# Kernel tuning notes

Measured on AMD Instinct MI355X. Metric: run time of the kernel, lower is better.

The kernel has to match this reference:

```python
import jax, jax.numpy as jnp
import numpy as np

N = 20000
DEG = 16
E = N * DEG
IN_DIM = 512
OUT_DIM = 512
H = 4
D = OUT_DIM // H            # head_dim = 128
POS_DIM = 3
M_ROPE = D // (POS_DIM * 2) # 21
D_ROPE = POS_DIM * 2 * M_ROPE  # 126 (2 trailing dims unrotated)
ROPE_BASE = 10000.0

INV_FREQ = jnp.exp(-jnp.arange(M_ROPE, dtype=jnp.float32) * (np.log(ROPE_BASE) / M_ROPE))


def _rope(t, pos):
    # t: (N, D, H), pos: (N, POS_DIM)
    n = t.shape[0]
    angles = pos[:, :, None] * INV_FREQ[None, None, :]        # (N, POS_DIM, M)
    cos = jnp.cos(angles)[..., None]                           # (N, POS_DIM, M, 1)
    sin = jnp.sin(angles)[..., None]
    part = t[:, :D_ROPE, :].reshape(n, POS_DIM, M_ROPE, 2, H)
    even, odd = part[..., 0, :], part[..., 1, :]
    rot_even = even * cos - odd * sin
    rot_odd = even * sin + odd * cos
    rot = jnp.stack((rot_even, rot_odd), axis=3).reshape(n, D_ROPE, H)
    return jnp.concatenate([rot, t[:, D_ROPE:, :]], axis=1)


def setup_inputs() -> dict:
    key = jax.random.key(0)
    ks = jax.random.split(key, 12)
    x = jax.random.normal(ks[0], (N, IN_DIM), jnp.float32)
    pos = jax.random.uniform(ks[1], (N, POS_DIM), jnp.float32) * 100.0
    rows = jnp.repeat(jnp.arange(N, dtype=jnp.int32), DEG)  # sorted, every node has DEG out-edges
    cols = jax.random.randint(ks[2], (E,), 0, N, dtype=jnp.int32)
    s = 1.0 / np.sqrt(IN_DIM)
    Wq = jax.random.normal(ks[3], (OUT_DIM, IN_DIM), jnp.float32) * s
    Wk = jax.random.normal(ks[4], (OUT_DIM, IN_DIM), jnp.float32) * s
    Wv = jax.random.normal(ks[5], (OUT_DIM, IN_DIM), jnp.float32) * s
    Wo = jax.random.normal(ks[6], (OUT_DIM, OUT_DIM), jnp.float32) * s
    bq = jax.random.normal(ks[7], (OUT_DIM,), jnp.float32) * 0.01
    bk = jax.random.normal(ks[8], (OUT_DIM,), jnp.float32) * 0.01
    bv = jax.random.normal(ks[9], (OUT_DIM,), jnp.float32) * 0.01
    bo = jax.random.normal(ks[10], (OUT_DIM,), jnp.float32) * 0.01
    return {"x": x, "pos": pos, "rows": rows, "cols": cols,
            "Wq": Wq, "bq": bq, "Wk": Wk, "bk": bk, "Wv": Wv, "bv": bv, "Wo": Wo, "bo": bo}


def reference(x, pos, rows, cols, Wq, bq, Wk, bk, Wv, bv, Wo, bo):
    n = x.shape[0]
    q = (x @ Wq.T + bq).reshape(n, D, H)
    k = (x @ Wk.T + bk).reshape(n, D, H)
    v = (x @ Wv.T + bv).reshape(n, D, H)
    # scaling by sqrt(k.size(1)) == sqrt(head_dim)
    q = q / jnp.sqrt(jnp.asarray(D, q.dtype))
    q = _rope(q, pos)
    k = _rope(k, pos)
    # per-edge scores: s[e,h] = sum_d q[rows[e],d,h] * k[cols[e],d,h]
    scores = jnp.einsum('edh,edh->eh', q[rows], k[cols])  # (E, H)
    # row-wise sparse softmax per head
    row_max = jax.ops.segment_max(scores, rows, num_segments=n, indices_are_sorted=True)
    p = jnp.exp(scores - row_max[rows])
    denom = jax.ops.segment_sum(p, rows, num_segments=n, indices_are_sorted=True)
    attn = p / denom[rows]                                 # (E, H)
    # bspmm: y[i,d,h] = sum_{e: rows[e]=i} attn[e,h] * v[cols[e],d,h]
    y = jax.ops.segment_sum(attn[:, None, :] * v[cols], rows, num_segments=n, indices_are_sorted=True)
    out = y.reshape(n, OUT_DIM) @ Wo.T + bo
    return out
```

## Files before the change

kernel.cpp:

```cpp
#include <hip/hip_runtime.h>
#include <hip/hip_bf16.h>

#define NN 20000
#define DEG 16
#define KD 512
#define OD 512
#define NH 4
#define DH 128
#define DROPE 126

#define BM 128
#define BN 128
#define BK 64

typedef unsigned short u16;
typedef unsigned int u32;
typedef __attribute__((ext_vector_type(8))) short short8;
typedef __attribute__((ext_vector_type(4))) float f32x4;

__device__ __forceinline__ float b2f(u16 u){ return __uint_as_float((u32)u << 16); }
__device__ __forceinline__ u16 f2b(float f){
  u32 x = __float_as_uint(f);
  return (u16)((x + 0x7fffu + ((x >> 16) & 1u)) >> 16);
}
__device__ __forceinline__ void up8(uint4 u, float* f){
  f[0]=__uint_as_float(u.x<<16); f[1]=__uint_as_float(u.x&0xffff0000u);
  f[2]=__uint_as_float(u.y<<16); f[3]=__uint_as_float(u.y&0xffff0000u);
  f[4]=__uint_as_float(u.z<<16); f[5]=__uint_as_float(u.z&0xffff0000u);
  f[6]=__uint_as_float(u.w<<16); f[7]=__uint_as_float(u.w&0xffff0000u);
}
__device__ __forceinline__ uint4 cvt8(const float* s){
  uint4 a = *(const uint4*)s;
  uint4 b = *(const uint4*)(s + 4);
  uint4 o;
  o.x = (u32)f2b(__uint_as_float(a.x)) | ((u32)f2b(__uint_as_float(a.y)) << 16);
  o.y = (u32)f2b(__uint_as_float(a.z)) | ((u32)f2b(__uint_as_float(a.w)) << 16);
  o.z = (u32)f2b(__uint_as_float(b.x)) | ((u32)f2b(__uint_as_float(b.y)) << 16);
  o.w = (u32)f2b(__uint_as_float(b.z)) | ((u32)f2b(__uint_as_float(b.w)) << 16);
  return o;
}

__device__ __forceinline__ void load_lds16(const u16* g, u16* l) {
  __builtin_amdgcn_global_load_lds(
      (const __attribute__((address_space(1))) void*)g,
      (__attribute__((address_space(3))) void*)l, 16, 0, 0);
}

struct ConvJob {
  const float* x;  u16* xb;
  const float* w[4]; u16* wb[4];
  const float* b[4]; u16* bb[4];
};
__global__ __launch_bounds__(256) void conv_all(ConvJob j) {
  const int b = blockIdx.x;
  if (b < 5000) {
    const int i8 = (b * 256 + threadIdx.x) * 8;
    *(uint4*)(j.xb + i8) = cvt8(j.x + i8);
  } else if (b < 5512) {
    const int t = b - 5000;
    const int wsel = t >> 7;
    const int i8 = ((t & 127) * 256 + threadIdx.x) * 8;
    *(uint4*)(j.wb[wsel] + i8) = cvt8(j.w[wsel] + i8);
  } else {
    const int vsel = threadIdx.x >> 6;
    const int i8 = (threadIdx.x & 63) * 8;
    *(uint4*)(j.bb[vsel] + i8) = cvt8(j.b[vsel] + i8);
  }
}

__global__ __launch_bounds__(256, 4) void gemm_k(
    const u16* __restrict__ A,
    const u16* __restrict__ W0, const u16* __restrict__ B0,
    const u16* __restrict__ W1, const u16* __restrict__ B1,
    const u16* __restrict__ W2, const u16* __restrict__ B2,
    const float* __restrict__ pos,
    u16* __restrict__ o0, u16* __restrict__ o1, void* __restrict__ o2,
    int M, int only2, int f32out)
{
  __shared__ __align__(16) char smem[36864];
  __shared__ float posS[BM*3];
  __shared__ float freqS[21];
  u16* As = (u16*)smem;
  u16* Bs = As + BM*BK;

  const int b = blockIdx.x;
  const int xcd = b & 7, rem = b >> 3;
  int rowT, colT, w;
  if (only2) {
    rowT = (rem >> 2)*8 + xcd; colT = rem & 3; w = 2;
  } else {
    rowT = (rem / 12)*8 + xcd; const int sub = rem % 12; colT = sub & 3; w = sub >> 2;
  }
  if (rowT*BM >= M) return;

  const int tid = threadIdx.x;
  const int wave = tid >> 6, lane = tid & 63;
  const int wr = wave >> 1, wc = wave & 1;
  const int lm = lane & 15, lq = lane >> 4;
  const u16* W  = (w == 0) ? W0 : ((w == 1) ? W1 : W2);
  const u16* Bi = (w == 0) ? B0 : ((w == 1) ? B1 : B2);
  const int mode = w;
  u16* outQK = (w == 0) ? o0 : o1;

  f32x4 acc[4][4];
  #pragma unroll
  for (int i = 0; i < 4; i++)
    #pragma unroll
    for (int jj = 0; jj < 4; jj++)
      acc[i][jj] = (f32x4){0.f, 0.f, 0.f, 0.f};

  if (mode < 2) {
    if (tid < BM) {
      int gr = rowT*BM + tid; if (gr >= M) gr = M - 1;
      posS[tid*3+0] = pos[gr*3+0];
      posS[tid*3+1] = pos[gr*3+1];
      posS[tid*3+2] = pos[gr*3+2];
    }
    if (tid >= BM && tid < BM + 21)
      freqS[tid - BM] = __expf(-(float)(tid - BM) * 0.43858763676077064f);
  }

  for (int kt = 0; kt < KD; kt += BK) {
    #pragma unroll
    for (int it = 0; it < 4; it++) {
      const int chunk = it*256 + wave*64 + lane;
      const int row = chunk >> 3, gseg = (chunk & 7) ^ (row & 7);
      int gr = rowT*BM + row; if (gr >= M) gr = M - 1;
      load_lds16(A + (size_t)gr*KD + kt + gseg*8,
                 As + (size_t)(it*256 + wave*64)*8);
    }
    #pragma unroll
    for (int it = 0; it < 4; it++) {
      const int chunk = it*256 + wave*64 + lane;
      const int row = chunk >> 3, gseg = (chunk & 7) ^ (row & 7);
      load_lds16(W + (size_t)(colT*BN + row)*KD + kt + gseg*8,
                 Bs + (size_t)(it*256 + wave*64)*8);
    }
    __syncthreads();
    #pragma unroll
    for (int kk = 0; kk < BK; kk += 32) {
      const int ks = kk >> 3;
      short8 af[4], bfr[4];
      #pragma unroll
      for (int i = 0; i < 4; i++) {
        const int ra = wr*64 + i*16 + lm;
        af[i] = *(const short8*)(As + (size_t)(ra*8 + ((ks + lq) ^ (ra & 7)))*8);
      }
      #pragma unroll
      for (int i = 0; i < 4; i++) {
        const int rb = wc*64 + i*16 + lm;
        bfr[i] = *(const short8*)(Bs + (size_t)(rb*8 + ((ks + lq) ^ (rb & 7)))*8);
      }
      #pragma unroll
      for (int mi = 0; mi < 4; mi++)
        #pragma unroll
        for (int ni = 0; ni < 4; ni++)
          acc[mi][ni] = __builtin_amdgcn_mfma_f32_16x16x32_bf16(af[mi], bfr[ni], acc[mi][ni], 0, 0, 0);
    }
    __syncthreads();
  }

  float bvv[4];
  #pragma unroll
  for (int ni = 0; ni < 4; ni++)
    bvv[ni] = b2f(Bi[colT*BN + wc*64 + ni*16 + lm]);

  u16* Cs = (u16*)smem;

  if (mode == 2 && f32out) {
    #pragma unroll
    for (int mi = 0; mi < 4; mi++)
      #pragma unroll
      for (int ni = 0; ni < 4; ni++) {
        const int Cg = colT*BN + wc*64 + ni*16 + lm;
        #pragma unroll
        for (int r = 0; r < 4; r++) {
          const int grow = rowT*BM + wr*64 + mi*16 + lq*4 + r;
          if (grow < M) ((float*)o2)[(size_t)grow*OD + Cg] = acc[mi][ni][r] + bvv[ni];
        }
      }
    return;
  }

  if (mode == 2) {
    #pragma unroll
    for (int mi = 0; mi < 4; mi++)
      #pragma unroll
      for (int ni = 0; ni < 4; ni++) {
        const int cloc = wc*64 + ni*16 + lm;
        #pragma unroll
        for (int r = 0; r < 4; r++) {
          const int rloc = wr*64 + mi*16 + lq*4 + r;
          Cs[rloc*136 + cloc] = f2b(acc[mi][ni][r] + bvv[ni]);
        }
      }
    __syncthreads();
    #pragma unroll
    for (int pass = 0; pass < 8; pass++) {
      const int c2 = pass*256 + tid;
      const int cc = c2 & 15, rloc = c2 >> 4;
      const int grow = rowT*BM + rloc;
      if (grow < M) {
        uint4 v = *(const uint4*)(Cs + rloc*136 + cc*8);
        *(uint4*)((u16*)o2 + (size_t)grow*OD + colT*BN + cc*8) = v;
      }
    }
    return;
  }

  #pragma unroll
  for (int mi = 0; mi < 4; mi++) {
    #pragma unroll
    for (int ni = 0; ni < 4; ni++) {
      const int cloc = wc*64 + ni*16 + lm;
      const int h = cloc & 3, dloc = cloc >> 2;
      const int d = colT*32 + dloc;
      #pragma unroll
      for (int r = 0; r < 4; r++) {
        const int rloc = wr*64 + mi*16 + lq*4 + r;
        float v = acc[mi][ni][r] + bvv[ni];
        if (mode == 0) v *= 0.08838834764831845f;
        const float partner = __shfl_xor(v, 4);
        float vr = v;
        if (d < DROPE) {
          const int pp = d / 42, rem2 = d - pp*42, m = rem2 >> 1, par = rem2 & 1;
          const float ang = posS[rloc*3 + pp] * freqS[m];
          float sn, cs; __sincosf(ang, &sn, &cs);
          vr = par ? (v*cs + partner*sn) : (v*cs - partner*sn);
        }
        Cs[rloc*144 + h*36 + dloc] = f2b(vr);
      }
    }
  }
  __syncthreads();
  #pragma unroll
  for (int pass = 0; pass < 8; pass++) {
    const int c2 = pass*256 + tid;
    const int dd8 = c2 & 3, h = (c2 >> 2) & 3, rloc = c2 >> 4;
    const int grow = rowT*BM + rloc;
    if (grow < M) {
      uint2 a = *(const uint2*)(Cs + rloc*144 + h*36 + dd8*8);
      uint2 b2 = *(const uint2*)(Cs + rloc*144 + h*36 + dd8*8 + 4);
      *(uint4*)(outQK + ((size_t)grow*NH + h)*DH + colT*32 + dd8*8)
          = make_uint4(a.x, a.y, b2.x, b2.y);
    }
  }
}

__global__ __launch_bounds__(256, 3) void edge_attn(
    const int* __restrict__ cols, const u16* __restrict__ qf,
    const u16* __restrict__ kf, const u16* __restrict__ vf,
    u16* __restrict__ y)
{
  const int wave = threadIdx.x >> 6;
  const int lane = threadIdx.x & 63;
  const int n = blockIdx.x*4 + wave;
  const int j = lane >> 2, h = lane & 3;
  const int col = cols[n*DEG + j];

  const uint4 qall = *(const uint4*)(qf + (size_t)n*OD + lane*8);

  int cjs[16];
  #pragma unroll
  for (int jj = 0; jj < 16; jj++) cjs[jj] = __shfl(col, jj*4);

  uint4 kreg[16];
  #pragma unroll
  for (int jj = 0; jj < 16; jj++)
    kreg[jj] = *(const uint4*)(kf + (size_t)cjs[jj]*OD + lane*8);

  uint4 vreg[16];
  #pragma unroll
  for (int jj = 0; jj < 16; jj++)
    vreg[jj] = *(const uint4*)(vf + (size_t)cjs[jj]*OD + lane*8);

  float qa[8];
  up8(qall, qa);

  float s = 0.f;
  #pragma unroll
  for (int jj = 0; jj < 16; jj++) {
    float ka[8];
    up8(kreg[jj], ka);
    float pr = qa[0]*ka[0] + qa[1]*ka[1] + qa[2]*ka[2] + qa[3]*ka[3]
             + qa[4]*ka[4] + qa[5]*ka[5] + qa[6]*ka[6] + qa[7]*ka[7];
    pr += __shfl_xor(pr, 1);
    pr += __shfl_xor(pr, 2);
    pr += __shfl_xor(pr, 4);
    pr += __shfl_xor(pr, 8);
    const float red = __shfl(pr, h*16);
    s = (j == jj) ? red : s;
  }

  float mx = s;
  #pragma unroll
  for (int msk = 4; msk < 64; msk <<= 1) mx = fmaxf(mx, __shfl_xor(mx, msk));
  float p = expf(s - mx);
  float dn = p;
  #pragma unroll
  for (int msk = 4; msk < 64; msk <<= 1) dn += __shfl_xor(dn, msk);
  const float attn = p / dn;

  float ya[8];
  #pragma unroll
  for (int t = 0; t < 8; t++) ya[t] = 0.f;
  #pragma unroll
  for (int jj = 0; jj < 16; jj++) {
    const float a0 = __shfl(attn, jj*4+0);
    const float a1 = __shfl(attn, jj*4+1);
    const float a2 = __shfl(attn, jj*4+2);
    const float a3 = __shfl(attn, jj*4+3);
    float va[8];
    up8(vreg[jj], va);
    ya[0] += a0*va[0]; ya[1] += a1*va[1]; ya[2] += a2*va[2]; ya[3] += a3*va[3];
    ya[4] += a0*va[4]; ya[5] += a1*va[5]; ya[6] += a2*va[6]; ya[7] += a3*va[7];
  }
  u32 pk[4];
  #pragma unroll
  for (int t = 0; t < 4; t++)
    pk[t] = (u32)f2b(ya[2*t]) | ((u32)f2b(ya[2*t+1]) << 16);
  *(uint4*)(y + (size_t)n*OD + lane*8) = make_uint4(pk[0], pk[1], pk[2], pk[3]);
}

extern "C" void kernel_launch(void* const* d_in, const int* in_sizes, int n_in,
                              void* d_out, int out_size, void* d_ws, size_t ws_size,
                              hipStream_t stream) {
  (void)in_sizes; (void)n_in; (void)out_size; (void)ws_size;
  const float* x   = (const float*)d_in[0];
  const float* pos = (const float*)d_in[1];
  const int* cols = (const int*)d_in[3];
  const float* Wq = (const float*)d_in[4];
  const float* bq = (const float*)d_in[5];
  const float* Wk = (const float*)d_in[6];
  const float* bk = (const float*)d_in[7];
  const float* Wv = (const float*)d_in[8];
  const float* bv = (const float*)d_in[9];
  const float* Wo = (const float*)d_in[10];
  const float* bo = (const float*)d_in[11];

  char* ws = (char*)d_ws;
  size_t off = 0;
  auto carve = [&](size_t bytes) { char* p = ws + off; off += (bytes + 15) & ~(size_t)15; return p; };
  u16* xb   = (u16*)carve((size_t)NN*KD*2);
  u16* Wqb  = (u16*)carve((size_t)OD*KD*2);
  u16* Wkb  = (u16*)carve((size_t)OD*KD*2);
  u16* Wvb  = (u16*)carve((size_t)OD*KD*2);
  u16* Wob  = (u16*)carve((size_t)OD*OD*2);
  u16* bqb  = (u16*)carve((size_t)OD*2);
  u16* bkb  = (u16*)carve((size_t)OD*2);
  u16* bvb  = (u16*)carve((size_t)OD*2);
  u16* bob  = (u16*)carve((size_t)OD*2);
  u16* qf   = (u16*)carve((size_t)NN*OD*2);
  u16* kf   = (u16*)carve((size_t)NN*OD*2);
  u16* vf   = (u16*)carve((size_t)NN*OD*2);
  u16* y    = (u16*)carve((size_t)NN*OD*2);

  ConvJob cj;
  cj.x = x; cj.xb = xb;
  cj.w[0]=Wq; cj.w[1]=Wk; cj.w[2]=Wv; cj.w[3]=Wo;
  cj.wb[0]=Wqb; cj.wb[1]=Wkb; cj.wb[2]=Wvb; cj.wb[3]=Wob;
  cj.b[0]=bq; cj.b[1]=bk; cj.b[2]=bv; cj.b[3]=bo;
  cj.bb[0]=bqb; cj.bb[1]=bkb; cj.bb[2]=bvb; cj.bb[3]=bob;
  conv_all<<<dim3(5513), 256, 0, stream>>>(cj);

  gemm_k<<<dim3(1920), 256, 0, stream>>>(xb, Wqb, bqb, Wkb, bkb, Wvb, bvb, pos,
                                         qf, kf, (void*)vf, NN, 0, 0);
  edge_attn<<<dim3(NN/4), 256, 0, stream>>>(cols, qf, kf, vf, y);
  gemm_k<<<dim3(640), 256, 0, stream>>>(y, Wqb, bqb, Wkb, bkb, Wob, bob, pos,
                                        qf, kf, d_out, NN, 1, 1);
}
```

Baseline: 255.6 us.

## Halve GEMM K-tile and split epilogue staging to raise occupancy

```diff
diff --git a/kernel.cpp b/kernel.cpp
--- a/kernel.cpp
+++ b/kernel.cpp
@@ -11,7 +11,7 @@
 
 #define BM 128
 #define BN 128
-#define BK 64
+#define BK 32
 
 typedef unsigned short u16;
 typedef unsigned int u32;
@@ -68,7 +68,7 @@
   }
 }
 
-__global__ __launch_bounds__(256, 4) void gemm_k(
+__global__ __launch_bounds__(256, 6) void gemm_k(
     const u16* __restrict__ A,
     const u16* __restrict__ W0, const u16* __restrict__ B0,
     const u16* __restrict__ W1, const u16* __restrict__ B1,
@@ -77,7 +77,7 @@
     u16* __restrict__ o0, u16* __restrict__ o1, void* __restrict__ o2,
     int M, int only2, int f32out)
 {
-  __shared__ __align__(16) char smem[36864];
+  __shared__ __align__(16) char smem[18432];
   __shared__ float posS[BM*3];
   __shared__ float freqS[21];
   u16* As = (u16*)smem;
@@ -122,41 +122,37 @@
 
   for (int kt = 0; kt < KD; kt += BK) {
     #pragma unroll
-    for (int it = 0; it < 4; it++) {
+    for (int it = 0; it < 2; it++) {
       const int chunk = it*256 + wave*64 + lane;
-      const int row = chunk >> 3, gseg = (chunk & 7) ^ (row & 7);
+      const int row = chunk >> 2, gseg = (chunk & 3) ^ (row & 3);
       int gr = rowT*BM + row; if (gr >= M) gr = M - 1;
       load_lds16(A + (size_t)gr*KD + kt + gseg*8,
                  As + (size_t)(it*256 + wave*64)*8);
     }
     #pragma unroll
-    for (int it = 0; it < 4; it++) {
+    for (int it = 0; it < 2; it++) {
       const int chunk = it*256 + wave*64 + lane;
-      const int row = chunk >> 3, gseg = (chunk & 7) ^ (row & 7);
+      const int row = chunk >> 2, gseg = (chunk & 3) ^ (row & 3);
       load_lds16(W + (size_t)(colT*BN + row)*KD + kt + gseg*8,
                  Bs + (size_t)(it*256 + wave*64)*8);
     }
     __syncthreads();
-    #pragma unroll
-    for (int kk = 0; kk < BK; kk += 32) {
-      const int ks = kk >> 3;
-      short8 af[4], bfr[4];
+    short8 af[4], bfr[4];
+    #pragma unroll
+    for (int i = 0; i < 4; i++) {
+      const int ra = wr*64 + i*16 + lm;
+      af[i] = *(const short8*)(As + (size_t)(ra*4 + (lq ^ (ra & 3)))*8);
+    }
+    #pragma unroll
+    for (int i = 0; i < 4; i++) {
+      const int rb = wc*64 + i*16 + lm;
+      bfr[i] = *(const short8*)(Bs + (size_t)(rb*4 + (lq ^ (rb & 3)))*8);
+    }
+    #pragma unroll
+    for (int mi = 0; mi < 4; mi++)
       #pragma unroll
-      for (int i = 0; i < 4; i++) {
-        const int ra = wr*64 + i*16 + lm;
-        af[i] = *(const short8*)(As + (size_t)(ra*8 + ((ks + lq) ^ (ra & 7)))*8);
-      }
-      #pragma unroll
-      for (int i = 0; i < 4; i++) {
-        const int rb = wc*64 + i*16 + lm;
-        bfr[i] = *(const short8*)(Bs + (size_t)(rb*8 + ((ks + lq) ^ (rb & 7)))*8);
-      }
-      #pragma unroll
-      for (int mi = 0; mi < 4; mi++)
-        #pragma unroll
-        for (int ni = 0; ni < 4; ni++)
-          acc[mi][ni] = __builtin_amdgcn_mfma_f32_16x16x32_bf16(af[mi], bfr[ni], acc[mi][ni], 0, 0, 0);
-    }
+      for (int ni = 0; ni < 4; ni++)
+        acc[mi][ni] = __builtin_amdgcn_mfma_f32_16x16x32_bf16(af[mi], bfr[ni], acc[mi][ni], 0, 0, 0);
     __syncthreads();
   }
 
@@ -184,66 +180,79 @@
 
   if (mode == 2) {
     #pragma unroll
-    for (int mi = 0; mi < 4; mi++)
+    for (int pass = 0; pass < 2; pass++) {
+      if (wr == pass) {
+        #pragma unroll
+        for (int mi = 0; mi < 4; mi++)
+          #pragma unroll
+          for (int ni = 0; ni < 4; ni++) {
+            const int cloc = wc*64 + ni*16 + lm;
+            #pragma unroll
+            for (int r = 0; r < 4; r++) {
+              const int rl = mi*16 + lq*4 + r;
+              Cs[rl*136 + cloc] = f2b(acc[mi][ni][r] + bvv[ni]);
+            }
+          }
+      }
+      __syncthreads();
       #pragma unroll
-      for (int ni = 0; ni < 4; ni++) {
-        const int cloc = wc*64 + ni*16 + lm;
+      for (int sp = 0; sp < 4; sp++) {
+        const int c2 = sp*256 + tid;
+        const int cc = c2 & 15, rl = c2 >> 4;
+        const int grow = rowT*BM + pass*64 + rl;
+        if (grow < M) {
+          uint4 v = *(const uint4*)(Cs + rl*136 + cc*8);
+          *(uint4*)((u16*)o2 + (size_t)grow*OD + colT*BN + cc*8) = v;
+        }
+      }
+      __syncthreads();
+    }
+    return;
+  }
+
+  #pragma unroll
+  for (int pass = 0; pass < 2; pass++) {
+    if (wr == pass) {
+      #pragma unroll
+      for (int mi = 0; mi < 4; mi++) {
         #pragma unroll
-        for (int r = 0; r < 4; r++) {
-          const int rloc = wr*64 + mi*16 + lq*4 + r;
-          Cs[rloc*136 + cloc] = f2b(acc[mi][ni][r] + bvv[ni]);
+        for (int ni = 0; ni < 4; ni++) {
+          const int cloc = wc*64 + ni*16 + lm;
+          const int h = cloc & 3, dloc = cloc >> 2;
+          const int d = colT*32 + dloc;
+          #pragma unroll
+          for (int r = 0; r < 4; r++) {
+            const int rl = mi*16 + lq*4 + r;
+            const int rloc = pass*64 + rl;
+            float v = acc[mi][ni][r] + bvv[ni];
+            if (mode == 0) v *= 0.08838834764831845f;
+            const float partner = __shfl_xor(v, 4);
+            float vr = v;
+            if (d < DROPE) {
+              const int pp = d / 42, rem2 = d - pp*42, m = rem2 >> 1, par = rem2 & 1;
+              const float ang = posS[rloc*3 + pp] * freqS[m];
+              float sn, cs; __sincosf(ang, &sn, &cs);
+              vr = par ? (v*cs + partner*sn) : (v*cs - partner*sn);
+            }
+            Cs[rl*144 + h*36 + dloc] = f2b(vr);
+          }
         }
       }
+    }
     __syncthreads();
     #pragma unroll
-    for (int pass = 0; pass < 8; pass++) {
-      const int c2 = pass*256 + tid;
-      const int cc = c2 & 15, rloc = c2 >> 4;
-      const int grow = rowT*BM + rloc;
+    for (int sp = 0; sp < 4; sp++) {
+      const int c2 = sp*256 + tid;
+      const int dd8 = c2 & 3, h = (c2 >> 2) & 3, rl = c2 >> 4;
+      const int grow = rowT*BM + pass*64 + rl;
       if (grow < M) {
-        uint4 v = *(const uint4*)(Cs + rloc*136 + cc*8);
-        *(uint4*)((u16*)o2 + (size_t)grow*OD + colT*BN + cc*8) = v;
-      }
-    }
-    return;
-  }
-
-  #pragma unroll
-  for (int mi = 0; mi < 4; mi++) {
-    #pragma unroll
-    for (int ni = 0; ni < 4; ni++) {
-      const int cloc = wc*64 + ni*16 + lm;
-      const int h = cloc & 3, dloc = cloc >> 2;
-      const int d = colT*32 + dloc;
-      #pragma unroll
-      for (int r = 0; r < 4; r++) {
-        const int rloc = wr*64 + mi*16 + lq*4 + r;
-        float v = acc[mi][ni][r] + bvv[ni];
-        if (mode == 0) v *= 0.08838834764831845f;
-        const float partner = __shfl_xor(v, 4);
-        float vr = v;
-        if (d < DROPE) {
-          const int pp = d / 42, rem2 = d - pp*42, m = rem2 >> 1, par = rem2 & 1;
-          const float ang = posS[rloc*3 + pp] * freqS[m];
-          float sn, cs; __sincosf(ang, &sn, &cs);
-          vr = par ? (v*cs + partner*sn) : (v*cs - partner*sn);
-        }
-        Cs[rloc*144 + h*36 + dloc] = f2b(vr);
-      }
-    }
-  }
-  __syncthreads();
-  #pragma unroll
-  for (int pass = 0; pass < 8; pass++) {
-    const int c2 = pass*256 + tid;
-    const int dd8 = c2 & 3, h = (c2 >> 2) & 3, rloc = c2 >> 4;
-    const int grow = rowT*BM + rloc;
-    if (grow < M) {
-      uint2 a = *(const uint2*)(Cs + rloc*144 + h*36 + dd8*8);
-      uint2 b2 = *(const uint2*)(Cs + rloc*144 + h*36 + dd8*8 + 4);
-      *(uint4*)(outQK + ((size_t)grow*NH + h)*DH + colT*32 + dd8*8)
-          = make_uint4(a.x, a.y, b2.x, b2.y);
-    }
+        uint2 a = *(const uint2*)(Cs + rl*144 + h*36 + dd8*8);
+        uint2 b2 = *(const uint2*)(Cs + rl*144 + h*36 + dd8*8 + 4);
+        *(uint4*)(outQK + ((size_t)grow*NH + h)*DH + colT*32 + dd8*8)
+            = make_uint4(a.x, a.y, b2.x, b2.y);
+      }
+    }
+    __syncthreads();
   }
 }
 
```

After: 507.8 us. +98.6%, slower.
